# Performance work log

Measured on AMD Instinct MI355X. Metric: run time of the kernel, lower is better.

The kernel has to match this reference:

```python
import jax, jax.numpy as jnp
import numpy as np

N_NODES = 50000
N_EDGES = 800000
N_PAIRS = 262144
F_IN, H1, H2, NCLS, HEADS = 572, 256, 128, 65, 2


def _bn(x, g, b, eps=1e-5):
    mu = x.mean(axis=0)
    var = x.var(axis=0)
    return g * (x - mu) * jax.lax.rsqrt(var + eps) + b


def _gat_conv(x, src, dst, W, a_src, a_dst, bias, heads, ch):
    """PyG GATConv, concat=False (mean over heads), negative_slope=0.2."""
    n = x.shape[0]
    h = (x @ W).reshape(n, heads, ch)                     # [N,H,C]
    s_n = (h * a_src[None]).sum(-1)                       # [N,H]
    d_n = (h * a_dst[None]).sum(-1)                       # [N,H]
    alpha = jax.nn.leaky_relu(s_n[src] + d_n[dst], 0.2)   # [E,H]
    m = jax.ops.segment_max(alpha, dst, num_segments=n)
    m = jnp.where(jnp.isfinite(m), m, 0.0)
    e = jnp.exp(alpha - m[dst])
    z = jax.ops.segment_sum(e, dst, num_segments=n)
    w = e / (z[dst] + 1e-16)                              # edge softmax per dst
    msg = h[src] * w[:, :, None]                          # [E,H,C]
    out = jax.ops.segment_sum(msg, dst, num_segments=n)   # [N,H,C]
    return out.mean(axis=1) + bias                        # concat=False -> mean


def setup_inputs() -> dict:
    key = jax.random.key(0)
    ks = jax.random.split(key, 24)
    g = lambda k, shp, fan: jax.random.normal(k, shp, jnp.float32) * (1.0 / np.sqrt(fan))
    inp = {
        "edge_index": jax.random.randint(ks[0], (2, N_EDGES), 0, N_NODES, jnp.int32),
        "x": jax.random.normal(ks[1], (N_NODES, F_IN), jnp.float32),
        "edge_id": jax.random.randint(ks[2], (2, N_PAIRS), 0, N_NODES, jnp.int32),
        "W1": g(ks[3], (F_IN, HEADS * H1), F_IN),
        "a_src1": g(ks[4], (HEADS, H1), H1),
        "a_dst1": g(ks[5], (HEADS, H1), H1),
        "b1": jnp.zeros((H1,), jnp.float32),
        "bn1_g": jnp.ones((H1,), jnp.float32), "bn1_b": jnp.zeros((H1,), jnp.float32),
        "W2": g(ks[6], (H1, HEADS * H1), H1),
        "a_src2": g(ks[7], (HEADS, H1), H1),
        "a_dst2": g(ks[8], (HEADS, H1), H1),
        "b2": jnp.zeros((H1,), jnp.float32),
        "bn2_g": jnp.ones((H1,), jnp.float32), "bn2_b": jnp.zeros((H1,), jnp.float32),
        "lw1": g(ks[9], (2 * H1, H2), 2 * H1), "lb1": jnp.zeros((H2,), jnp.float32),
        "bn3_g": jnp.ones((H2,), jnp.float32), "bn3_b": jnp.zeros((H2,), jnp.float32),
        "lw2": g(ks[10], (H2, H2), H2), "lb2": jnp.zeros((H2,), jnp.float32),
        "bn4_g": jnp.ones((H2,), jnp.float32), "bn4_b": jnp.zeros((H2,), jnp.float32),
        "fw": g(ks[11], (H2, NCLS), H2), "fb": jnp.zeros((NCLS,), jnp.float32),
    }
    return inp


def reference(edge_index, x, edge_id,
              W1, a_src1, a_dst1, b1, bn1_g, bn1_b,
              W2, a_src2, a_dst2, b2, bn2_g, bn2_b,
              lw1, lb1, bn3_g, bn3_b,
              lw2, lb2, bn4_g, bn4_b,
              fw, fb):
    n = x.shape[0]
    # PyG GATConv default add_self_loops=True
    loops = jnp.arange(n, dtype=edge_index.dtype)
    src = jnp.concatenate([edge_index[0], loops])
    dst = jnp.concatenate([edge_index[1], loops])

    h = _gat_conv(x, src, dst, W1, a_src1, a_dst1, b1, HEADS, H1)
    h = jax.nn.relu(_bn(h, bn1_g, bn1_b))
    h = _gat_conv(h, src, dst, W2, a_src2, a_dst2, b2, HEADS, H1)
    h = jax.nn.relu(_bn(h, bn2_g, bn2_b))

    pair = jnp.concatenate([h[edge_id[0]], h[edge_id[1]]], axis=1)  # [P, 2*H1]
    z = jax.nn.relu(_bn(pair @ lw1 + lb1, bn3_g, bn3_b))
    z = jax.nn.relu(_bn(z @ lw2 + lb2, bn4_g, bn4_b))
    return z @ fw + fb
```

## Files before the change

kernel.cpp:

```cpp
#include <hip/hip_runtime.h>

constexpr int NN = 50000;
constexpr int NE = 800000;
constexpr int NP = 262144;
constexpr int ET = NE + NN;

using short8 = __attribute__((ext_vector_type(8))) short;
using f32x4  = __attribute__((ext_vector_type(4))) float;

__device__ __forceinline__ ushort f2b(float f) {
  unsigned u = __float_as_uint(f);
  return (ushort)((u + 0x7FFFu + ((u >> 16) & 1u)) >> 16);
}
__device__ __forceinline__ float b2f(ushort b) {
  return __uint_as_float(((unsigned)b) << 16);
}

template<bool GATHER, bool OUT_BF16, bool STATS>
__global__ __launch_bounds__(256)
void mfma_gemm(const ushort* __restrict__ A, const ushort* __restrict__ BT,
               void* __restrict__ Cp, int M, int N, int Kpad, int Cld,
               const float* __restrict__ bias,
               const int* __restrict__ idx0, const int* __restrict__ idx1,
               double* __restrict__ stats)
{
  __shared__ __align__(16) ushort As[128 * 40];
  __shared__ __align__(16) ushort Bs[128 * 40];
  __shared__ int idxs[256];
  const int tid = threadIdx.x;
  const int lane = tid & 63;
  const int wave = tid >> 6;
  const int row0 = blockIdx.y * 128, col0 = blockIdx.x * 128;
  const int wm = (wave >> 1) * 64, wn = (wave & 1) * 64;
  const int lrow = lane & 15, lk = (lane >> 4) * 8;

  if constexpr (GATHER) {
    if (tid < 128) {
      int r = row0 + tid;
      idxs[tid]       = (r < M) ? idx0[r] : 0;
      idxs[128 + tid] = (r < M) ? idx1[r] : 0;
    }
    __syncthreads();
  }

  f32x4 acc[4][4];
  #pragma unroll
  for (int i = 0; i < 4; ++i)
    #pragma unroll
    for (int j = 0; j < 4; ++j)
      acc[i][j] = (f32x4){0.f, 0.f, 0.f, 0.f};

  for (int kt = 0; kt < Kpad; kt += 32) {
    #pragma unroll
    for (int c = tid; c < 512; c += 256) {
      int m = c >> 2, c8 = c & 3;
      int r = row0 + m;
      int kk = kt + c8 * 8;
      uint4 v = {0u, 0u, 0u, 0u};
      if (r < M) {
        const ushort* sp;
        if (GATHER) {
          int node = (kk < 256) ? idxs[m] : idxs[128 + m];
          sp = A + (size_t)node * 256 + (kk & 255);
        } else {
          sp = A + (size_t)r * Kpad + kk;
        }
        v = *(const uint4*)sp;
      }
      *(uint4*)(As + m * 40 + c8 * 8) = v;
    }
    #pragma unroll
    for (int c = tid; c < 512; c += 256) {
      int n = c >> 2, c8 = c & 3;
      *(uint4*)(Bs + n * 40 + c8 * 8) =
          *(const uint4*)(BT + (size_t)(col0 + n) * Kpad + kt + c8 * 8);
    }
    __syncthreads();

    short8 af[4], bfr[4];
    #pragma unroll
    for (int i = 0; i < 4; ++i)
      af[i] = *(const short8*)(As + (wm + i * 16 + lrow) * 40 + lk);
    #pragma unroll
    for (int j = 0; j < 4; ++j)
      bfr[j] = *(const short8*)(Bs + (wn + j * 16 + lrow) * 40 + lk);
    #pragma unroll
    for (int i = 0; i < 4; ++i)
      #pragma unroll
      for (int j = 0; j < 4; ++j)
        acc[i][j] = __builtin_amdgcn_mfma_f32_16x16x32_bf16(af[i], bfr[j],
                                                            acc[i][j], 0, 0, 0);
    __syncthreads();
  }

  float* sacc = (float*)As;
  if constexpr (STATS) {
    sacc[tid] = 0.f;
    __syncthreads();
  }
  float cs[4] = {0.f, 0.f, 0.f, 0.f}, cq[4] = {0.f, 0.f, 0.f, 0.f};
  #pragma unroll
  for (int i = 0; i < 4; ++i) {
    int r0 = row0 + wm + i * 16 + (lane >> 4) * 4;
    #pragma unroll
    for (int j = 0; j < 4; ++j) {
      int col = col0 + wn + j * 16 + lrow;
      if (col >= N) continue;
      float bv = bias ? bias[col] : 0.f;
      #pragma unroll
      for (int rg = 0; rg < 4; ++rg) {
        int row = r0 + rg;
        if (row >= M) continue;
        float val = acc[i][j][rg] + bv;
        if (OUT_BF16)
          ((ushort*)Cp)[(size_t)row * Cld + col] = f2b(val);
        else
          ((float*)Cp)[(size_t)row * Cld + col] = val;
        if (STATS) { cs[j] += val; cq[j] += val * val; }
      }
    }
  }
  if constexpr (STATS) {
    #pragma unroll
    for (int j = 0; j < 4; ++j) {
      int cl = wn + j * 16 + lrow;
      atomicAdd(&sacc[2 * cl + 0], cs[j]);
      atomicAdd(&sacc[2 * cl + 1], cq[j]);
    }
    __syncthreads();
    if (tid < 128) {
      unsafeAtomicAdd(&stats[tid],       (double)sacc[2 * tid + 0]);
      unsafeAtomicAdd(&stats[128 + tid], (double)sacc[2 * tid + 1]);
    }
  }
}

__global__ void prep_weights(const float* __restrict__ W1, ushort* __restrict__ W1T,
                             const float* __restrict__ W2, ushort* __restrict__ W2T,
                             const float* __restrict__ lw1, ushort* __restrict__ LW1T,
                             const float* __restrict__ lw2, ushort* __restrict__ LW2T,
                             const float* __restrict__ fw, ushort* __restrict__ FWT)
{
  int i = blockIdx.x * blockDim.x + threadIdx.x;
  const float* W; ushort* BT; int K, N, Kpad;
  if (i < 294912)      { W = W1;  BT = W1T;  K = 572; N = 512; Kpad = 576; }
  else if (i < 425984) { i -= 294912; W = W2;  BT = W2T;  K = 256; N = 512; Kpad = 256; }
  else if (i < 491520) { i -= 425984; W = lw1; BT = LW1T; K = 512; N = 128; Kpad = 512; }
  else if (i < 507904) { i -= 491520; W = lw2; BT = LW2T; K = 128; N = 128; Kpad = 128; }
  else                 { i -= 507904; W = fw;  BT = FWT;  K = 128; N = 65;  Kpad = 128; }
  int n = i / Kpad, k = i % Kpad;
  float v = (n < N && k < K) ? W[(size_t)k * N + n] : 0.f;
  BT[i] = f2b(v);
}

__global__ void conv_x(const float* __restrict__ x, ushort* __restrict__ xb)
{
  int i = blockIdx.x * blockDim.x + threadIdx.x;
  if (i >= NN * 144) return;
  int r = i / 144, c4 = (i % 144) * 4;
  ushort4 o = {0, 0, 0, 0};
  if (c4 < 572) {
    float4 v = *(const float4*)(x + (size_t)r * 572 + c4);
    o.x = f2b(v.x); o.y = f2b(v.y); o.z = f2b(v.z); o.w = f2b(v.w);
  }
  *(ushort4*)(xb + (size_t)r * 576 + c4) = o;
}

__global__ void deg_count(const int* __restrict__ ei, int* __restrict__ deg)
{
  int e = blockIdx.x * blockDim.x + threadIdx.x;
  if (e >= ET) return;
  int dst = (e < NE) ? ei[NE + e] : e - NE;
  atomicAdd(&deg[dst], 1);
}

__global__ __launch_bounds__(1024)
void scan_deg(const int* __restrict__ deg, int* __restrict__ rowptr,
              int* __restrict__ cursor)
{
  __shared__ int tot[1024];
  const int t = threadIdx.x;
  const int CH = (NN + 1023) / 1024;
  const int base = t * CH;
  int s = 0;
  for (int i = 0; i < CH; ++i) {
    int idx = base + i;
    if (idx < NN) s += deg[idx];
  }
  tot[t] = s;
  __syncthreads();
  for (int off = 1; off < 1024; off <<= 1) {
    int v = (t >= off) ? tot[t - off] : 0;
    __syncthreads();
    tot[t] += v;
    __syncthreads();
  }
  int run = (t == 0) ? 0 : tot[t - 1];
  for (int i = 0; i < CH; ++i) {
    int idx = base + i;
    if (idx <= NN) { rowptr[idx] = run; if (idx < NN) cursor[idx] = run; }
    if (idx < NN) run += deg[idx];
  }
}

__global__ void scatter_edges(const int* __restrict__ ei, int* __restrict__ cursor,
                              int* __restrict__ csr_src)
{
  int e = blockIdx.x * blockDim.x + threadIdx.x;
  if (e >= ET) return;
  int src, dst;
  if (e < NE) { src = ei[e]; dst = ei[NE + e]; }
  else        { src = dst = e - NE; }
  int pos = atomicAdd(&cursor[dst], 1);
  csr_src[pos] = src;
}


__global__ void node_coeffs(const ushort* __restrict__ hb,
                            const float* __restrict__ a_src,
                            const float* __restrict__ a_dst,
                            float* __restrict__ s_n, float* __restrict__ d_n)
{
  int node = (blockIdx.x * blockDim.x + threadIdx.x) >> 6;
  int lane = threadIdx.x & 63;
  if (node >= NN) return;
  int head = lane >> 5;
  int cidx = (lane * 8) & 255;
  short8 hv = *(const short8*)(hb + (size_t)node * 512 + lane * 8);
  float4 a0 = *(const float4*)(a_src + head * 256 + cidx);
  float4 a1 = *(const float4*)(a_src + head * 256 + cidx + 4);
  float4 d0 = *(const float4*)(a_dst + head * 256 + cidx);
  float4 d1 = *(const float4*)(a_dst + head * 256 + cidx + 4);
  float h0 = b2f((ushort)hv[0]), h1 = b2f((ushort)hv[1]);
  float h2 = b2f((ushort)hv[2]), h3 = b2f((ushort)hv[3]);
  float h4 = b2f((ushort)hv[4]), h5 = b2f((ushort)hv[5]);
  float h6 = b2f((ushort)hv[6]), h7 = b2f((ushort)hv[7]);
  float ss = h0*a0.x + h1*a0.y + h2*a0.z + h3*a0.w
           + h4*a1.x + h5*a1.y + h6*a1.z + h7*a1.w;
  float dd = h0*d0.x + h1*d0.y + h2*d0.z + h3*d0.w
           + h4*d1.x + h5*d1.y + h6*d1.z + h7*d1.w;
  #pragma unroll
  for (int off = 16; off > 0; off >>= 1) {
    ss += __shfl_xor(ss, off);
    dd += __shfl_xor(dd, off);
  }
  if ((lane & 31) == 0) {
    s_n[node * 2 + head] = ss;
    d_n[node * 2 + head] = dd;
  }
}

__global__ __launch_bounds__(256)
void gat_aggregate(const int* __restrict__ rowptr, const int* __restrict__ csr_src,
                   const ushort* __restrict__ hb,
                   const float* __restrict__ s_n, const float* __restrict__ d_n,
                   const float* __restrict__ bias, float* __restrict__ outp,
                   double* __restrict__ stats)
{
  __shared__ float sacc[512];
  sacc[threadIdx.x] = 0.f;
  sacc[256 + threadIdx.x] = 0.f;
  __syncthreads();

  const int wave = threadIdx.x >> 6, lane = threadIdx.x & 63;
  const int base = blockIdx.x * 16 + wave * 4;
  const float4 bb = *(const float4*)(bias + lane * 4);
  const float2* sn2 = (const float2*)s_n;

  for (int n = 0; n < 4; ++n) {
    const int dst = base + n;
    if (dst < NN) {
      const int beg = rowptr[dst], end = rowptr[dst + 1];
      const float d0 = d_n[dst * 2 + 0], d1 = d_n[dst * 2 + 1];

      float m0 = -1e30f, m1 = -1e30f;
      for (int i = beg + lane; i < end; i += 64) {
        float2 sv = sn2[csr_src[i]];
        float a0 = sv.x + d0; a0 = a0 > 0.f ? a0 : 0.2f * a0;
        float a1 = sv.y + d1; a1 = a1 > 0.f ? a1 : 0.2f * a1;
        m0 = fmaxf(m0, a0); m1 = fmaxf(m1, a1);
      }
      #pragma unroll
      for (int off = 32; off > 0; off >>= 1) {
        m0 = fmaxf(m0, __shfl_xor(m0, off));
        m1 = fmaxf(m1, __shfl_xor(m1, off));
      }

      float z0 = 0.f, z1 = 0.f;
      for (int i = beg + lane; i < end; i += 64) {
        float2 sv = sn2[csr_src[i]];
        float a0 = sv.x + d0; a0 = a0 > 0.f ? a0 : 0.2f * a0;
        float a1 = sv.y + d1; a1 = a1 > 0.f ? a1 : 0.2f * a1;
        z0 += __expf(a0 - m0);
        z1 += __expf(a1 - m1);
      }
      #pragma unroll
      for (int off = 32; off > 0; off >>= 1) {
        z0 += __shfl_xor(z0, off);
        z1 += __shfl_xor(z1, off);
      }
      const float rz0 = 1.f / (z0 + 1e-16f);
      const float rz1 = 1.f / (z1 + 1e-16f);

      float4 acc0 = {0.f, 0.f, 0.f, 0.f};
      float4 acc1 = {0.f, 0.f, 0.f, 0.f};
      int i = beg;
      for (; i + 2 <= end; i += 2) {
        int sA = csr_src[i], sB = csr_src[i + 1];
        const ushort4 uA0 = *(const ushort4*)(hb + (size_t)sA * 512 + lane * 4);
        const ushort4 uA1 = *(const ushort4*)(hb + (size_t)sA * 512 + 256 + lane * 4);
        const ushort4 uB0 = *(const ushort4*)(hb + (size_t)sB * 512 + lane * 4);
        const ushort4 uB1 = *(const ushort4*)(hb + (size_t)sB * 512 + 256 + lane * 4);
        float2 svA = sn2[sA], svB = sn2[sB];
        float aA0 = svA.x + d0; aA0 = aA0 > 0.f ? aA0 : 0.2f * aA0;
        float aA1 = svA.y + d1; aA1 = aA1 > 0.f ? aA1 : 0.2f * aA1;
        float aB0 = svB.x + d0; aB0 = aB0 > 0.f ? aB0 : 0.2f * aB0;
        float aB1 = svB.y + d1; aB1 = aB1 > 0.f ? aB1 : 0.2f * aB1;
        float wA0 = __expf(aA0 - m0) * rz0, wA1 = __expf(aA1 - m1) * rz1;
        float wB0 = __expf(aB0 - m0) * rz0, wB1 = __expf(aB1 - m1) * rz1;
        acc0.x = fmaf(b2f(uA0.x), wA0, acc0.x); acc0.y = fmaf(b2f(uA0.y), wA0, acc0.y);
        acc0.z = fmaf(b2f(uA0.z), wA0, acc0.z); acc0.w = fmaf(b2f(uA0.w), wA0, acc0.w);
        acc1.x = fmaf(b2f(uA1.x), wA1, acc1.x); acc1.y = fmaf(b2f(uA1.y), wA1, acc1.y);
        acc1.z = fmaf(b2f(uA1.z), wA1, acc1.z); acc1.w = fmaf(b2f(uA1.w), wA1, acc1.w);
        acc0.x = fmaf(b2f(uB0.x), wB0, acc0.x); acc0.y = fmaf(b2f(uB0.y), wB0, acc0.y);
        acc0.z = fmaf(b2f(uB0.z), wB0, acc0.z); acc0.w = fmaf(b2f(uB0.w), wB0, acc0.w);
        acc1.x = fmaf(b2f(uB1.x), wB1, acc1.x); acc1.y = fmaf(b2f(uB1.y), wB1, acc1.y);
        acc1.z = fmaf(b2f(uB1.z), wB1, acc1.z); acc1.w = fmaf(b2f(uB1.w), wB1, acc1.w);
      }
      if (i < end) {
        int s = csr_src[i];
        float2 sv = sn2[s];
        float a0 = sv.x + d0; a0 = a0 > 0.f ? a0 : 0.2f * a0;
        float a1 = sv.y + d1; a1 = a1 > 0.f ? a1 : 0.2f * a1;
        float w0 = __expf(a0 - m0) * rz0;
        float w1 = __expf(a1 - m1) * rz1;
        ushort4 u0 = *(const ushort4*)(hb + (size_t)s * 512 + lane * 4);
        ushort4 u1 = *(const ushort4*)(hb + (size_t)s * 512 + 256 + lane * 4);
        acc0.x = fmaf(b2f(u0.x), w0, acc0.x); acc0.y = fmaf(b2f(u0.y), w0, acc0.y);
        acc0.z = fmaf(b2f(u0.z), w0, acc0.z); acc0.w = fmaf(b2f(u0.w), w0, acc0.w);
        acc1.x = fmaf(b2f(u1.x), w1, acc1.x); acc1.y = fmaf(b2f(u1.y), w1, acc1.y);
        acc1.z = fmaf(b2f(u1.z), w1, acc1.z); acc1.w = fmaf(b2f(u1.w), w1, acc1.w);
      }

      float4 o;
      o.x = 0.5f * (acc0.x + acc1.x) + bb.x;
      o.y = 0.5f * (acc0.y + acc1.y) + bb.y;
      o.z = 0.5f * (acc0.z + acc1.z) + bb.z;
      o.w = 0.5f * (acc0.w + acc1.w) + bb.w;
      *(float4*)(outp + (size_t)dst * 256 + lane * 4) = o;

      const int c = lane * 4;
      atomicAdd(&sacc[c + 0], o.x);       atomicAdd(&sacc[c + 1], o.y);
      atomicAdd(&sacc[c + 2], o.z);       atomicAdd(&sacc[c + 3], o.w);
      atomicAdd(&sacc[256 + c + 0], o.x * o.x);
      atomicAdd(&sacc[256 + c + 1], o.y * o.y);
      atomicAdd(&sacc[256 + c + 2], o.z * o.z);
      atomicAdd(&sacc[256 + c + 3], o.w * o.w);
    }
  }
  __syncthreads();
  const int c = threadIdx.x;
  unsafeAtomicAdd(&stats[c],       (double)sacc[c]);
  unsafeAtomicAdd(&stats[256 + c], (double)sacc[256 + c]);
}

__global__ void bn_apply_relu_b4(const float* __restrict__ x, ushort* __restrict__ y,
                                 const double* __restrict__ stats,
                                 const float* __restrict__ g, const float* __restrict__ b,
                                 int total4, int cols, float inv_rows)
{
  int i = blockIdx.x * blockDim.x + threadIdx.x;
  if (i >= total4) return;
  int base = i * 4;
  int c = base % cols;
  float4 xv = *(const float4*)(x + base);
  float4 gv = *(const float4*)(g + c);
  float4 bv = *(const float4*)(b + c);
  ushort4 o;
  #pragma unroll
  for (int k = 0; k < 4; ++k) {
    float mean = (float)(stats[c + k] * (double)inv_rows);
    float var = (float)(stats[cols + c + k] * (double)inv_rows) - mean * mean;
    float sc = ((const float*)&gv)[k] * rsqrtf(var + 1e-5f);
    float sh = ((const float*)&bv)[k] - mean * sc;
    float v = fmaxf(fmaf(((const float*)&xv)[k], sc, sh), 0.f);
    ((ushort*)&o)[k] = f2b(v);
  }
  *(ushort4*)(y + base) = o;
}

static void gat_layer(const ushort* ain, int Kpad, const ushort* WT,
                      const float* asrc, const float* adst, const float* bias,
                      const float* bng, const float* bnb,
                      const int* rowptr, const int* csr_src,
                      ushort* hb, float* t, ushort* featb,
                      float* s_n, float* d_n, double* stats, hipStream_t st)
{
  dim3 b256(256);
  mfma_gemm<false, true, false><<<dim3(4, 391), b256, 0, st>>>(
      ain, WT, hb, NN, 512, Kpad, 512, nullptr, nullptr, nullptr, nullptr);
  node_coeffs<<<(NN + 3) / 4, b256, 0, st>>>(hb, asrc, adst, s_n, d_n);
  gat_aggregate<<<(NN + 15) / 16, b256, 0, st>>>(rowptr, csr_src, hb,
                                                 s_n, d_n, bias, t, stats);
  bn_apply_relu_b4<<<(NN * 64 + 255) / 256, b256, 0, st>>>(
      t, featb, stats, bng, bnb, NN * 64, 256, 1.0f / NN);
}

extern "C" void kernel_launch(void* const* d_in, const int* in_sizes, int n_in,
                              void* d_out, int out_size, void* d_ws, size_t ws_size,
                              hipStream_t stream)
{
  const int*   edge_index = (const int*)d_in[0];
  const float* x      = (const float*)d_in[1];
  const int*   edge_id = (const int*)d_in[2];
  const float* W1     = (const float*)d_in[3];
  const float* a_src1 = (const float*)d_in[4];
  const float* a_dst1 = (const float*)d_in[5];
  const float* b1     = (const float*)d_in[6];
  const float* bn1_g  = (const float*)d_in[7];
  const float* bn1_b  = (const float*)d_in[8];
  const float* W2     = (const float*)d_in[9];
  const float* a_src2 = (const float*)d_in[10];
  const float* a_dst2 = (const float*)d_in[11];
  const float* b2     = (const float*)d_in[12];
  const float* bn2_g  = (const float*)d_in[13];
  const float* bn2_b  = (const float*)d_in[14];
  const float* lw1    = (const float*)d_in[15];
  const float* lb1    = (const float*)d_in[16];
  const float* bn3_g  = (const float*)d_in[17];
  const float* bn3_b  = (const float*)d_in[18];
  const float* lw2    = (const float*)d_in[19];
  const float* lb2    = (const float*)d_in[20];
  const float* bn4_g  = (const float*)d_in[21];
  const float* bn4_b  = (const float*)d_in[22];
  const float* fw     = (const float*)d_in[23];
  const float* fb     = (const float*)d_in[24];
  float* out = (float*)d_out;

  char* w = (char*)d_ws;
  ushort* xb     = (ushort*)(w + 0);
  ushort* hb     = (ushort*)(w + 57600000);
  float*  t_buf  = (float*)(w + 108800000);
  ushort* feat1b = (ushort*)(w + 160000000);
  ushort* feat2b = (ushort*)(w + 185600000);
  float*  z1     = (float*)(w + 0);
  ushort* z1b    = (ushort*)(w + 160000000);
  float*  z2     = (float*)(w + 0);
  ushort* z2b    = (ushort*)(w + 227108864);
  int*    csr_src = (int*)(w + 294217728);
  int*    deg     = (int*)(w + 297700000);
  int*    rowptr  = (int*)(w + 297900000);
  int*    cursor  = (int*)(w + 298100008);
  float*  s_n     = (float*)(w + 298300008);
  float*  d_n     = (float*)(w + 298700008);
  double* stats   = (double*)(w + 299100008);
  ushort* W1T     = (ushort*)(w + 300000000);
  ushort* W2T     = (ushort*)(w + 300600000);
  ushort* LW1T    = (ushort*)(w + 300900000);
  ushort* LW2T    = (ushort*)(w + 301040000);
  ushort* FWT     = (ushort*)(w + 301080000);

  double* st1 = stats,        *st2 = stats + 512;
  double* st3 = stats + 1024, *st4 = stats + 1536;

  dim3 b256(256);

  hipMemsetAsync(stats, 0, 4 * 512 * sizeof(double), stream);

  prep_weights<<<2048, b256, 0, stream>>>(W1, W1T, W2, W2T, lw1, LW1T,
                                          lw2, LW2T, fw, FWT);
  conv_x<<<(NN * 144 + 255) / 256, b256, 0, stream>>>(x, xb);

  hipMemsetAsync(deg, 0, NN * sizeof(int), stream);
  deg_count<<<(ET + 255) / 256, b256, 0, stream>>>(edge_index, deg);
  scan_deg<<<1, 1024, 0, stream>>>(deg, rowptr, cursor);
  scatter_edges<<<(ET + 255) / 256, b256, 0, stream>>>(edge_index, cursor, csr_src);

  gat_layer(xb, 576, W1T, a_src1, a_dst1, b1, bn1_g, bn1_b, rowptr, csr_src,
            hb, t_buf, feat1b, s_n, d_n, st1, stream);
  gat_layer(feat1b, 256, W2T, a_src2, a_dst2, b2, bn2_g, bn2_b, rowptr, csr_src,
            hb, t_buf, feat2b, s_n, d_n, st2, stream);

  mfma_gemm<true, false, true><<<dim3(1, 2048), b256, 0, stream>>>(
      feat2b, LW1T, z1, NP, 128, 512, 128, lb1, edge_id, edge_id + NP, st3);
  bn_apply_relu_b4<<<(NP * 32 + 255) / 256, b256, 0, stream>>>(
      z1, z1b, st3, bn3_g, bn3_b, NP * 32, 128, 1.0f / NP);
  mfma_gemm<false, false, true><<<dim3(1, 2048), b256, 0, stream>>>(
      z1b, LW2T, z2, NP, 128, 128, 128, lb2, nullptr, nullptr, st4);
  bn_apply_relu_b4<<<(NP * 32 + 255) / 256, b256, 0, stream>>>(
      z2, z2b, st4, bn4_g, bn4_b, NP * 32, 128, 1.0f / NP);
  mfma_gemm<false, false, false><<<dim3(1, 2048), b256, 0, stream>>>(
      z2b, FWT, out, NP, 65, 128, 65, fb, nullptr, nullptr, nullptr);
}
```

Measured before the change: 1.464 ms.

## Project nodes before pair gather, degree-sort aggregation, and store intermediates in bf16

The pair MLP's first layer is split algebraically. Each node's features are projected once by the two halves of lw1 (a 50000x256 GEMM), and each pair is then formed by a gather-add in a new pair_add kernel. This replaces the 262144-row gathered GEMM with K=512. GAT aggregation now visits destinations in a degree-sorted order built from a histogram permutation. Nodes with at most 64 edges use a single-pass wave softmax, and each lane handles 8 channels of one head. Intermediate activations (GAT outputs and the z1/z2 pair buffers) are stored as bf16 instead of fp32, with the BN-apply step done in place. This cuts memory traffic but adds rounding before the batch-norm statistics are applied.

```diff
diff --git a/kernel.cpp b/kernel.cpp
--- a/kernel.cpp
+++ b/kernel.cpp
@@ -15,18 +15,17 @@
 __device__ __forceinline__ float b2f(ushort b) {
   return __uint_as_float(((unsigned)b) << 16);
 }
-
-template<bool GATHER, bool OUT_BF16, bool STATS>
+__device__ __forceinline__ float lrelu(float a) { return a > 0.f ? a : 0.2f * a; }
+
+template<bool OUT_BF16, bool STATS>
 __global__ __launch_bounds__(256)
 void mfma_gemm(const ushort* __restrict__ A, const ushort* __restrict__ BT,
                void* __restrict__ Cp, int M, int N, int Kpad, int Cld,
                const float* __restrict__ bias,
-               const int* __restrict__ idx0, const int* __restrict__ idx1,
                double* __restrict__ stats)
 {
   __shared__ __align__(16) ushort As[128 * 40];
   __shared__ __align__(16) ushort Bs[128 * 40];
-  __shared__ int idxs[256];
   const int tid = threadIdx.x;
   const int lane = tid & 63;
   const int wave = tid >> 6;
@@ -34,15 +33,6 @@
   const int wm = (wave >> 1) * 64, wn = (wave & 1) * 64;
   const int lrow = lane & 15, lk = (lane >> 4) * 8;
 
-  if constexpr (GATHER) {
-    if (tid < 128) {
-      int r = row0 + tid;
-      idxs[tid]       = (r < M) ? idx0[r] : 0;
-      idxs[128 + tid] = (r < M) ? idx1[r] : 0;
-    }
-    __syncthreads();
-  }
-
   f32x4 acc[4][4];
   #pragma unroll
   for (int i = 0; i < 4; ++i)
@@ -57,16 +47,7 @@
       int r = row0 + m;
       int kk = kt + c8 * 8;
       uint4 v = {0u, 0u, 0u, 0u};
-      if (r < M) {
-        const ushort* sp;
-        if (GATHER) {
-          int node = (kk < 256) ? idxs[m] : idxs[128 + m];
-          sp = A + (size_t)node * 256 + (kk & 255);
-        } else {
-          sp = A + (size_t)r * Kpad + kk;
-        }
-        v = *(const uint4*)sp;
-      }
+      if (r < M) v = *(const uint4*)(A + (size_t)r * Kpad + kk);
       *(uint4*)(As + m * 40 + c8 * 8) = v;
     }
     #pragma unroll
@@ -137,20 +118,36 @@
 
 __global__ void prep_weights(const float* __restrict__ W1, ushort* __restrict__ W1T,
                              const float* __restrict__ W2, ushort* __restrict__ W2T,
-                             const float* __restrict__ lw1, ushort* __restrict__ LW1T,
+                             const float* __restrict__ lw1, ushort* __restrict__ PWT,
                              const float* __restrict__ lw2, ushort* __restrict__ LW2T,
-                             const float* __restrict__ fw, ushort* __restrict__ FWT)
+                             const float* __restrict__ fw, ushort* __restrict__ FWT,
+                             const float* __restrict__ lb1, float* __restrict__ biasP)
 {
   int i = blockIdx.x * blockDim.x + threadIdx.x;
-  const float* W; ushort* BT; int K, N, Kpad;
-  if (i < 294912)      { W = W1;  BT = W1T;  K = 572; N = 512; Kpad = 576; }
-  else if (i < 425984) { i -= 294912; W = W2;  BT = W2T;  K = 256; N = 512; Kpad = 256; }
-  else if (i < 491520) { i -= 425984; W = lw1; BT = LW1T; K = 512; N = 128; Kpad = 512; }
-  else if (i < 507904) { i -= 491520; W = lw2; BT = LW2T; K = 128; N = 128; Kpad = 128; }
-  else                 { i -= 507904; W = fw;  BT = FWT;  K = 128; N = 65;  Kpad = 128; }
-  int n = i / Kpad, k = i % Kpad;
-  float v = (n < N && k < K) ? W[(size_t)k * N + n] : 0.f;
-  BT[i] = f2b(v);
+  if (i >= 524544) return;
+  if (i >= 524288) {
+    int c = i - 524288;
+    biasP[c] = (c < 128) ? lb1[c] : 0.f;
+    return;
+  }
+  if (i < 294912) {
+    int n = i / 576, k = i % 576;
+    W1T[i] = f2b((k < 572) ? W1[(size_t)k * 512 + n] : 0.f);
+  } else if (i < 425984) {
+    int j = i - 294912; int n = j / 256, k = j % 256;
+    W2T[j] = f2b(W2[(size_t)k * 512 + n]);
+  } else if (i < 491520) {
+    int j = i - 425984; int n = j / 256, k = j % 256;
+    float v = (n < 128) ? lw1[(size_t)k * 128 + n]
+                        : lw1[(size_t)(k + 256) * 128 + (n - 128)];
+    PWT[j] = f2b(v);
+  } else if (i < 507904) {
+    int j = i - 491520; int n = j / 128, k = j % 128;
+    LW2T[j] = f2b(lw2[(size_t)k * 128 + n]);
+  } else {
+    int j = i - 507904; int n = j / 128, k = j % 128;
+    FWT[j] = f2b((n < 65) ? fw[(size_t)k * 65 + n] : 0.f);
+  }
 }
 
 __global__ void conv_x(const float* __restrict__ x, ushort* __restrict__ xb)
@@ -215,6 +212,39 @@
   csr_src[pos] = src;
 }
 
+__global__ void deg_hist(const int* __restrict__ deg, int* __restrict__ hist)
+{
+  int n = blockIdx.x * blockDim.x + threadIdx.x;
+  if (n >= NN) return;
+  int d = deg[n]; if (d > 255) d = 255;
+  atomicAdd(&hist[255 - d], 1);
+}
+
+__global__ void scan_hist(const int* __restrict__ hist, int* __restrict__ hcur)
+{
+  __shared__ int sh[256];
+  int t = threadIdx.x;
+  int v0 = hist[t];
+  sh[t] = v0;
+  __syncthreads();
+  for (int off = 1; off < 256; off <<= 1) {
+    int v = (t >= off) ? sh[t - off] : 0;
+    __syncthreads();
+    sh[t] += v;
+    __syncthreads();
+  }
+  hcur[t] = sh[t] - v0;
+}
+
+__global__ void build_perm(const int* __restrict__ deg, int* __restrict__ hcur,
+                           int* __restrict__ perm)
+{
+  int n = blockIdx.x * blockDim.x + threadIdx.x;
+  if (n >= NN) return;
+  int d = deg[n]; if (d > 255) d = 255;
+  int pos = atomicAdd(&hcur[255 - d], 1);
+  perm[pos] = n;
+}
 
 __global__ void node_coeffs(const ushort* __restrict__ hb,
                             const float* __restrict__ a_src,
@@ -251,10 +281,11 @@
 }
 
 __global__ __launch_bounds__(256)
-void gat_aggregate(const int* __restrict__ rowptr, const int* __restrict__ csr_src,
+void gat_aggregate(const int* __restrict__ perm,
+                   const int* __restrict__ rowptr, const int* __restrict__ csr_src,
                    const ushort* __restrict__ hb,
                    const float* __restrict__ s_n, const float* __restrict__ d_n,
-                   const float* __restrict__ bias, float* __restrict__ outp,
+                   const float* __restrict__ bias, ushort* __restrict__ outp,
                    double* __restrict__ stats)
 {
   __shared__ float sacc[512];
@@ -264,35 +295,90 @@
 
   const int wave = threadIdx.x >> 6, lane = threadIdx.x & 63;
   const int base = blockIdx.x * 16 + wave * 4;
-  const float4 bb = *(const float4*)(bias + lane * 4);
+  const bool hi = lane >= 32;
+  const int ch0 = (lane & 31) * 8;
+  const float4 bba = *(const float4*)(bias + ch0);
+  const float4 bbb = *(const float4*)(bias + ch0 + 4);
+  const float bias8[8] = {bba.x, bba.y, bba.z, bba.w, bbb.x, bbb.y, bbb.z, bbb.w};
   const float2* sn2 = (const float2*)s_n;
 
+  float ssum[8] = {0,0,0,0,0,0,0,0}, ssq[8] = {0,0,0,0,0,0,0,0};
+
   for (int n = 0; n < 4; ++n) {
-    const int dst = base + n;
-    if (dst < NN) {
-      const int beg = rowptr[dst], end = rowptr[dst + 1];
-      const float d0 = d_n[dst * 2 + 0], d1 = d_n[dst * 2 + 1];
-
+    const int idx = base + n;
+    if (idx >= NN) continue;
+    const int dst = perm[idx];
+    const int beg = rowptr[dst], end = rowptr[dst + 1];
+    const int cnt = end - beg;
+    const float d0 = d_n[dst * 2 + 0], d1 = d_n[dst * 2 + 1];
+
+    float acc[8] = {0,0,0,0,0,0,0,0};
+
+    if (cnt <= 64) {
+      float a0 = -1e30f, a1 = -1e30f;
+      if (lane < cnt) {
+        float2 sv = sn2[csr_src[beg + lane]];
+        a0 = lrelu(sv.x + d0);
+        a1 = lrelu(sv.y + d1);
+      }
+      float m0 = a0, m1 = a1;
+      #pragma unroll
+      for (int off = 32; off > 0; off >>= 1) {
+        m0 = fmaxf(m0, __shfl_xor(m0, off));
+        m1 = fmaxf(m1, __shfl_xor(m1, off));
+      }
+      float ez0 = (lane < cnt) ? __expf(a0 - m0) : 0.f;
+      float ez1 = (lane < cnt) ? __expf(a1 - m1) : 0.f;
+      float z0 = ez0, z1 = ez1;
+      #pragma unroll
+      for (int off = 32; off > 0; off >>= 1) {
+        z0 += __shfl_xor(z0, off);
+        z1 += __shfl_xor(z1, off);
+      }
+      const float rz0 = 1.f / (z0 + 1e-16f);
+      const float rz1 = 1.f / (z1 + 1e-16f);
+
+      int li = 0;
+      for (; li + 2 <= cnt; li += 2) {
+        int sA = csr_src[beg + li], sB = csr_src[beg + li + 1];
+        short8 hA = *(const short8*)(hb + (size_t)sA * 512 + lane * 8);
+        short8 hB = *(const short8*)(hb + (size_t)sB * 512 + lane * 8);
+        float wA0 = __shfl(ez0, li) * rz0,     wA1 = __shfl(ez1, li) * rz1;
+        float wB0 = __shfl(ez0, li + 1) * rz0, wB1 = __shfl(ez1, li + 1) * rz1;
+        float wA = hi ? wA1 : wA0;
+        float wB = hi ? wB1 : wB0;
+        #pragma unroll
+        for (int k = 0; k < 8; ++k) {
+          acc[k] = fmaf(b2f((ushort)hA[k]), wA, acc[k]);
+          acc[k] = fmaf(b2f((ushort)hB[k]), wB, acc[k]);
+        }
+      }
+      if (li < cnt) {
+        int sA = csr_src[beg + li];
+        short8 hA = *(const short8*)(hb + (size_t)sA * 512 + lane * 8);
+        float wA0 = __shfl(ez0, li) * rz0, wA1 = __shfl(ez1, li) * rz1;
+        float wA = hi ? wA1 : wA0;
+        #pragma unroll
+        for (int k = 0; k < 8; ++k)
+          acc[k] = fmaf(b2f((ushort)hA[k]), wA, acc[k]);
+      }
+    } else {
       float m0 = -1e30f, m1 = -1e30f;
       for (int i = beg + lane; i < end; i += 64) {
         float2 sv = sn2[csr_src[i]];
-        float a0 = sv.x + d0; a0 = a0 > 0.f ? a0 : 0.2f * a0;
-        float a1 = sv.y + d1; a1 = a1 > 0.f ? a1 : 0.2f * a1;
-        m0 = fmaxf(m0, a0); m1 = fmaxf(m1, a1);
+        m0 = fmaxf(m0, lrelu(sv.x + d0));
+        m1 = fmaxf(m1, lrelu(sv.y + d1));
       }
       #pragma unroll
       for (int off = 32; off > 0; off >>= 1) {
         m0 = fmaxf(m0, __shfl_xor(m0, off));
         m1 = fmaxf(m1, __shfl_xor(m1, off));
       }
-
       float z0 = 0.f, z1 = 0.f;
       for (int i = beg + lane; i < end; i += 64) {
         float2 sv = sn2[csr_src[i]];
-        float a0 = sv.x + d0; a0 = a0 > 0.f ? a0 : 0.2f * a0;
-        float a1 = sv.y + d1; a1 = a1 > 0.f ? a1 : 0.2f * a1;
-        z0 += __expf(a0 - m0);
-        z1 += __expf(a1 - m1);
+        z0 += __expf(lrelu(sv.x + d0) - m0);
+        z1 += __expf(lrelu(sv.y + d1) - m1);
       }
       #pragma unroll
       for (int off = 32; off > 0; off >>= 1) {
@@ -301,61 +387,41 @@
       }
       const float rz0 = 1.f / (z0 + 1e-16f);
       const float rz1 = 1.f / (z1 + 1e-16f);
-
-      float4 acc0 = {0.f, 0.f, 0.f, 0.f};
-      float4 acc1 = {0.f, 0.f, 0.f, 0.f};
-      int i = beg;
-      for (; i + 2 <= end; i += 2) {
-        int sA = csr_src[i], sB = csr_src[i + 1];
-        const ushort4 uA0 = *(const ushort4*)(hb + (size_t)sA * 512 + lane * 4);
-        const ushort4 uA1 = *(const ushort4*)(hb + (size_t)sA * 512 + 256 + lane * 4);
-        const ushort4 uB0 = *(const ushort4*)(hb + (size_t)sB * 512 + lane * 4);
-        const ushort4 uB1 = *(const ushort4*)(hb + (size_t)sB * 512 + 256 + lane * 4);
-        float2 svA = sn2[sA], svB = sn2[sB];
-        float aA0 = svA.x + d0; aA0 = aA0 > 0.f ? aA0 : 0.2f * aA0;
-        float aA1 = svA.y + d1; aA1 = aA1 > 0.f ? aA1 : 0.2f * aA1;
-        float aB0 = svB.x + d0; aB0 = aB0 > 0.f ? aB0 : 0.2f * aB0;
-        float aB1 = svB.y + d1; aB1 = aB1 > 0.f ? aB1 : 0.2f * aB1;
-        float wA0 = __expf(aA0 - m0) * rz0, wA1 = __expf(aA1 - m1) * rz1;
-        float wB0 = __expf(aB0 - m0) * rz0, wB1 = __expf(aB1 - m1) * rz1;
-        acc0.x = fmaf(b2f(uA0.x), wA0, acc0.x); acc0.y = fmaf(b2f(uA0.y), wA0, acc0.y);
-        acc0.z = fmaf(b2f(uA0.z), wA0, acc0.z); acc0.w = fmaf(b2f(uA0.w), wA0, acc0.w);
-        acc1.x = fmaf(b2f(uA1.x), wA1, acc1.x); acc1.y = fmaf(b2f(uA1.y), wA1, acc1.y);
-        acc1.z = fmaf(b2f(uA1.z), wA1, acc1.z); acc1.w = fmaf(b2f(uA1.w), wA1, acc1.w);
-        acc0.x = fmaf(b2f(uB0.x), wB0, acc0.x); acc0.y = fmaf(b2f(uB0.y), wB0, acc0.y);
-        acc0.z = fmaf(b2f(uB0.z), wB0, acc0.z); acc0.w = fmaf(b2f(uB0.w), wB0, acc0.w);
-        acc1.x = fmaf(b2f(uB1.x), wB1, acc1.x); acc1.y = fmaf(b2f(uB1.y), wB1, acc1.y);
-        acc1.z = fmaf(b2f(uB1.z), wB1, acc1.z); acc1.w = fmaf(b2f(uB1.w), wB1, acc1.w);
-      }
-      if (i < end) {
+      for (int i = beg; i < end; ++i) {
         int s = csr_src[i];
         float2 sv = sn2[s];
-        float a0 = sv.x + d0; a0 = a0 > 0.f ? a0 : 0.2f * a0;
-        float a1 = sv.y + d1; a1 = a1 > 0.f ? a1 : 0.2f * a1;
-        float w0 = __expf(a0 - m0) * rz0;
-        float w1 = __expf(a1 - m1) * rz1;
-        ushort4 u0 = *(const ushort4*)(hb + (size_t)s * 512 + lane * 4);
-        ushort4 u1 = *(const ushort4*)(hb + (size_t)s * 512 + 256 + lane * 4);
-        acc0.x = fmaf(b2f(u0.x), w0, acc0.x); acc0.y = fmaf(b2f(u0.y), w0, acc0.y);
-        acc0.z = fmaf(b2f(u0.z), w0, acc0.z); acc0.w = fmaf(b2f(u0.w), w0, acc0.w);
-        acc1.x = fmaf(b2f(u1.x), w1, acc1.x); acc1.y = fmaf(b2f(u1.y), w1, acc1.y);
-        acc1.z = fmaf(b2f(u1.z), w1, acc1.z); acc1.w = fmaf(b2f(u1.w), w1, acc1.w);
-      }
-
-      float4 o;
-      o.x = 0.5f * (acc0.x + acc1.x) + bb.x;
-      o.y = 0.5f * (acc0.y + acc1.y) + bb.y;
-      o.z = 0.5f * (acc0.z + acc1.z) + bb.z;
-      o.w = 0.5f * (acc0.w + acc1.w) + bb.w;
-      *(float4*)(outp + (size_t)dst * 256 + lane * 4) = o;
-
-      const int c = lane * 4;
-      atomicAdd(&sacc[c + 0], o.x);       atomicAdd(&sacc[c + 1], o.y);
-      atomicAdd(&sacc[c + 2], o.z);       atomicAdd(&sacc[c + 3], o.w);
-      atomicAdd(&sacc[256 + c + 0], o.x * o.x);
-      atomicAdd(&sacc[256 + c + 1], o.y * o.y);
-      atomicAdd(&sacc[256 + c + 2], o.z * o.z);
-      atomicAdd(&sacc[256 + c + 3], o.w * o.w);
+        float w0 = __expf(lrelu(sv.x + d0) - m0) * rz0;
+        float w1 = __expf(lrelu(sv.y + d1) - m1) * rz1;
+        float w = hi ? w1 : w0;
+        short8 hv = *(const short8*)(hb + (size_t)s * 512 + lane * 8);
+        #pragma unroll
+        for (int k = 0; k < 8; ++k)
+          acc[k] = fmaf(b2f((ushort)hv[k]), w, acc[k]);
+      }
+    }
+
+    float ov[8];
+    #pragma unroll
+    for (int k = 0; k < 8; ++k)
+      ov[k] = 0.5f * (acc[k] + __shfl_xor(acc[k], 32)) + bias8[k];
+
+    ushort* op = outp + (size_t)dst * 256 + ch0;
+    if (!hi) {
+      ushort4 o = {f2b(ov[0]), f2b(ov[1]), f2b(ov[2]), f2b(ov[3])};
+      *(ushort4*)op = o;
+      #pragma unroll
+      for (int k = 0; k < 8; ++k) { ssum[k] += ov[k]; ssq[k] += ov[k] * ov[k]; }
+    } else {
+      ushort4 o = {f2b(ov[4]), f2b(ov[5]), f2b(ov[6]), f2b(ov[7])};
+      *(ushort4*)(op + 4) = o;
+    }
+  }
+
+  if (!hi) {
+    #pragma unroll
+    for (int k = 0; k < 8; ++k) {
+      atomicAdd(&sacc[ch0 + k], ssum[k]);
+      atomicAdd(&sacc[256 + ch0 + k], ssq[k]);
     }
   }
   __syncthreads();
@@ -364,16 +430,45 @@
   unsafeAtomicAdd(&stats[256 + c], (double)sacc[256 + c]);
 }
 
-__global__ void bn_apply_relu_b4(const float* __restrict__ x, ushort* __restrict__ y,
-                                 const double* __restrict__ stats,
-                                 const float* __restrict__ g, const float* __restrict__ b,
-                                 int total4, int cols, float inv_rows)
+__global__ __launch_bounds__(256)
+void pair_add(const ushort* __restrict__ P, const int* __restrict__ id0,
+              const int* __restrict__ id1, ushort* __restrict__ z1b,
+              double* __restrict__ stats)
+{
+  __shared__ float sacc[256];
+  sacc[threadIdx.x] = 0.f;
+  __syncthreads();
+  const int wave = threadIdx.x >> 6, lane = threadIdx.x & 63;
+  const int c = lane * 2;
+  const int pbase = blockIdx.x * 128 + wave * 32;
+  float s0 = 0.f, s1 = 0.f, q0 = 0.f, q1 = 0.f;
+  for (int k = 0; k < 32; ++k) {
+    int p = pbase + k;
+    int a = id0[p], b = id1[p];
+    ushort2 ua = *(const ushort2*)(P + (size_t)a * 256 + c);
+    ushort2 ub = *(const ushort2*)(P + (size_t)b * 256 + 128 + c);
+    float zx = b2f(ua.x) + b2f(ub.x);
+    float zy = b2f(ua.y) + b2f(ub.y);
+    ushort2 o = {f2b(zx), f2b(zy)};
+    *(ushort2*)(z1b + (size_t)p * 128 + c) = o;
+    s0 += zx; s1 += zy; q0 += zx * zx; q1 += zy * zy;
+  }
+  atomicAdd(&sacc[c], s0);       atomicAdd(&sacc[c + 1], s1);
+  atomicAdd(&sacc[128 + c], q0); atomicAdd(&sacc[128 + c + 1], q1);
+  __syncthreads();
+  unsafeAtomicAdd(&stats[threadIdx.x], (double)sacc[threadIdx.x]);
+}
+
+__global__ void bn_apply_b(const ushort* __restrict__ xin, ushort* __restrict__ y,
+                           const double* __restrict__ stats,
+                           const float* __restrict__ g, const float* __restrict__ b,
+                           int total4, int cols, float inv_rows)
 {
   int i = blockIdx.x * blockDim.x + threadIdx.x;
   if (i >= total4) return;
   int base = i * 4;
   int c = base % cols;
-  float4 xv = *(const float4*)(x + base);
+  ushort4 xv = *(const ushort4*)(xin + base);
   float4 gv = *(const float4*)(g + c);
   float4 bv = *(const float4*)(b + c);
   ushort4 o;
@@ -383,7 +478,7 @@
     float var = (float)(stats[cols + c + k] * (double)inv_rows) - mean * mean;
     float sc = ((const float*)&gv)[k] * rsqrtf(var + 1e-5f);
     float sh = ((const float*)&bv)[k] - mean * sc;
-    float v = fmaxf(fmaf(((const float*)&xv)[k], sc, sh), 0.f);
+    float v = fmaxf(fmaf(b2f(((const ushort*)&xv)[k]), sc, sh), 0.f);
     ((ushort*)&o)[k] = f2b(v);
   }
   *(ushort4*)(y + base) = o;
@@ -392,18 +487,18 @@
 static void gat_layer(const ushort* ain, int Kpad, const ushort* WT,
                       const float* asrc, const float* adst, const float* bias,
                       const float* bng, const float* bnb,
-                      const int* rowptr, const int* csr_src,
-                      ushort* hb, float* t, ushort* featb,
+                      const int* perm, const int* rowptr, const int* csr_src,
+                      ushort* hb, ushort* tb, ushort* featb,
                       float* s_n, float* d_n, double* stats, hipStream_t st)
 {
   dim3 b256(256);
-  mfma_gemm<false, true, false><<<dim3(4, 391), b256, 0, st>>>(
-      ain, WT, hb, NN, 512, Kpad, 512, nullptr, nullptr, nullptr, nullptr);
+  mfma_gemm<true, false><<<dim3(4, 391), b256, 0, st>>>(
+      ain, WT, hb, NN, 512, Kpad, 512, nullptr, nullptr);
   node_coeffs<<<(NN + 3) / 4, b256, 0, st>>>(hb, asrc, adst, s_n, d_n);
-  gat_aggregate<<<(NN + 15) / 16, b256, 0, st>>>(rowptr, csr_src, hb,
-                                                 s_n, d_n, bias, t, stats);
-  bn_apply_relu_b4<<<(NN * 64 + 255) / 256, b256, 0, st>>>(
-      t, featb, stats, bng, bnb, NN * 64, 256, 1.0f / NN);
+  gat_aggregate<<<(NN + 15) / 16, b256, 0, st>>>(perm, rowptr, csr_src, hb,
+                                                 s_n, d_n, bias, tb, stats);
+  bn_apply_b<<<(NN * 64 + 255) / 256, b256, 0, st>>>(
+      tb, featb, stats, bng, bnb, NN * 64, 256, 1.0f / NN);
 }
 
 extern "C" void kernel_launch(void* const* d_in, const int* in_sizes, int n_in,
@@ -440,13 +535,12 @@
   char* w = (char*)d_ws;
   ushort* xb     = (ushort*)(w + 0);
   ushort* hb     = (ushort*)(w + 57600000);
-  float*  t_buf  = (float*)(w + 108800000);
+  ushort* tb     = (ushort*)(w + 108800000);
   ushort* feat1b = (ushort*)(w + 160000000);
   ushort* feat2b = (ushort*)(w + 185600000);
-  float*  z1     = (float*)(w + 0);
-  ushort* z1b    = (ushort*)(w + 160000000);
-  float*  z2     = (float*)(w + 0);
-  ushort* z2b    = (ushort*)(w + 227108864);
+  ushort* z1b    = (ushort*)(w + 0);
+  ushort* Pbuf   = (ushort*)(w + 70000000);
+  ushort* z2b    = (ushort*)(w + 100000000);
   int*    csr_src = (int*)(w + 294217728);
   int*    deg     = (int*)(w + 297700000);
   int*    rowptr  = (int*)(w + 297900000);
@@ -454,11 +548,15 @@
   float*  s_n     = (float*)(w + 298300008);
   float*  d_n     = (float*)(w + 298700008);
   double* stats   = (double*)(w + 299100008);
+  int*    hist    = (int*)(w + 299150000);
+  int*    hcur    = (int*)(w + 299151024);
+  int*    perm    = (int*)(w + 299160000);
   ushort* W1T     = (ushort*)(w + 300000000);
   ushort* W2T     = (ushort*)(w + 300600000);
-  ushort* LW1T    = (ushort*)(w + 300900000);
+  ushort* PWT     = (ushort*)(w + 300900000);
   ushort* LW2T    = (ushort*)(w + 301040000);
   ushort* FWT     = (ushort*)(w + 301080000);
+  float*  biasP   = (float*)(w + 301200000);
 
   double* st1 = stats,        *st2 = stats + 512;
   double* st3 = stats + 1024, *st4 = stats + 1536;
@@ -466,29 +564,34 @@
   dim3 b256(256);
 
   hipMemsetAsync(stats, 0, 4 * 512 * sizeof(double), stream);
-
-  prep_weights<<<2048, b256, 0, stream>>>(W1, W1T, W2, W2T, lw1, LW1T,
-                                          lw2, LW2T, fw, FWT);
+  hipMemsetAsync(hist, 0, 256 * sizeof(int), stream);
+  hipMemsetAsync(deg, 0, NN * sizeof(int), stream);
+
+  prep_weights<<<(524544 + 255) / 256, b256, 0, stream>>>(
+      W1, W1T, W2, W2T, lw1, PWT, lw2, LW2T, fw, FWT, lb1, biasP);
   conv_x<<<(NN * 144 + 255) / 256, b256, 0, stream>>>(x, xb);
 
-  hipMemsetAsync(deg, 0, NN * sizeof(int), stream);
   deg_count<<<(ET + 255) / 256, b256, 0, stream>>>(edge_index, deg);
   scan_deg<<<1, 1024, 0, stream>>>(deg, rowptr, cursor);
   scatter_edges<<<(ET + 255) / 256, b256, 0, stream>>>(edge_index, cursor, csr_src);
-
-  gat_layer(xb, 576, W1T, a_src1, a_dst1, b1, bn1_g, bn1_b, rowptr, csr_src,
-            hb, t_buf, feat1b, s_n, d_n, st1, stream);
-  gat_layer(feat1b, 256, W2T, a_src2, a_dst2, b2, bn2_g, bn2_b, rowptr, csr_src,
-            hb, t_buf, feat2b, s_n, d_n, st2, stream);
-
-  mfma_gemm<true, false, true><<<dim3(1, 2048), b256, 0, stream>>>(
-      feat2b, LW1T, z1, NP, 128, 512, 128, lb1, edge_id, edge_id + NP, st3);
-  bn_apply_relu_b4<<<(NP * 32 + 255) / 256, b256, 0, stream>>>(
-      z1, z1b, st3, bn3_g, bn3_b, NP * 32, 128, 1.0f / NP);
-  mfma_gemm<false, false, true><<<dim3(1, 2048), b256, 0, stream>>>(
-      z1b, LW2T, z2, NP, 128, 128, 128, lb2, nullptr, nullptr, st4);
-  bn_apply_relu_b4<<<(NP * 32 + 255) / 256, b256, 0, stream>>>(
-      z2, z2b, st4, bn4_g, bn4_b, NP * 32, 128, 1.0f / NP);
-  mfma_gemm<false, false, false><<<dim3(1, 2048), b256, 0, stream>>>(
-      z2b, FWT, out, NP, 65, 128, 65, fb, nullptr, nullptr, nullptr);
-}
+  deg_hist<<<(NN + 255) / 256, b256, 0, stream>>>(deg, hist);
+  scan_hist<<<1, 256, 0, stream>>>(hist, hcur);
+  build_perm<<<(NN + 255) / 256, b256, 0, stream>>>(deg, hcur, perm);
+
+  gat_layer(xb, 576, W1T, a_src1, a_dst1, b1, bn1_g, bn1_b, perm, rowptr, csr_src,
+            hb, tb, feat1b, s_n, d_n, st1, stream);
+  gat_layer(feat1b, 256, W2T, a_src2, a_dst2, b2, bn2_g, bn2_b, perm, rowptr, csr_src,
+            hb, tb, feat2b, s_n, d_n, st2, stream);
+
+  mfma_gemm<true, false><<<dim3(2, 391), b256, 0, stream>>>(
+      feat2b, PWT, Pbuf, NN, 256, 256, 256, biasP, nullptr);
+  pair_add<<<NP / 128, b256, 0, stream>>>(Pbuf, edge_id, edge_id + NP, z1b, st3);
+  bn_apply_b<<<(NP * 32 + 255) / 256, b256, 0, stream>>>(
+      z1b, z1b, st3, bn3_g, bn3_b, NP * 32, 128, 1.0f / NP);
+  mfma_gemm<true, true><<<dim3(1, 2048), b256, 0, stream>>>(
+      z1b, LW2T, z2b, NP, 128, 128, 128, lb2, st4);
+  bn_apply_b<<<(NP * 32 + 255) / 256, b256, 0, stream>>>(
+      z2b, z2b, st4, bn4_g, bn4_b, NP * 32, 128, 1.0f / NP);
+  mfma_gemm<false, false><<<dim3(1, 2048), b256, 0, stream>>>(
+      z2b, FWT, out, NP, 65, 128, 65, fb, nullptr);
+}
```

Result: slower. 1.742 ms (+19.0%).
